# Optimization experiments

Measured on AMD Instinct MI355X. Metric: run time of the kernel, lower is better.

Reference implementation:

```python
import jax, jax.numpy as jnp
import numpy as np

NEG_POS_RATIO = 3
BETA = 1.0
ALPHA = 2.0


def _smooth_ex_loss(pred, tgt):
    # a = beta / (1 - exp(-alpha)); c = a - beta - beta/alpha
    a = BETA / (1.0 - np.exp(-ALPHA))
    c = a - BETA - BETA / ALPHA
    diff = jnp.abs(pred - tgt)
    return jnp.where(diff < 1.0,
                     a * (diff + (jnp.exp(-ALPHA * diff) - 1.0) / ALPHA),
                     BETA * diff + c)


def setup_inputs() -> dict:
    key = jax.random.key(0)
    k1, k2, k3, k4 = jax.random.split(key, 4)
    B, P, C = 128, 8732, 21
    return {
        "confidence": jax.random.normal(k1, (B, P, C), dtype=jnp.float32),
        "predicted_locations": jax.random.normal(k2, (B, P, 4), dtype=jnp.float32),
        "labels": jax.random.randint(k3, (B, P), 0, C, dtype=jnp.int64),
        "gt_locations": jax.random.normal(k4, (B, P, 4), dtype=jnp.float32),
    }


def reference(confidence, predicted_locations, labels, gt_locations):
    # confidence: [B, P, C]; labels: [B, P]; locations: [B, P, 4]
    logp = jax.nn.log_softmax(confidence, axis=2)
    pos_mask = labels > 0

    # --- hard negative mining (no-grad in original) ---
    bg_loss = jax.lax.stop_gradient(-logp[:, :, 0])          # [B, P]
    num_pos = pos_mask.sum(axis=1, keepdims=True)             # [B, 1]
    num_neg = num_pos * NEG_POS_RATIO
    mined = jnp.where(pos_mask, -jnp.inf, bg_loss)
    idx = jnp.argsort(-mined, axis=1)                         # descending sort
    orders = jnp.argsort(idx, axis=1)                         # rank of each prior
    neg_mask = orders < num_neg
    mask = pos_mask | neg_mask                                # [B, P]

    # --- classification loss: sum of CE over mined priors ---
    per_elem_ce = -jnp.take_along_axis(logp, labels[..., None], axis=2)[..., 0]
    classification_loss = jnp.sum(jnp.where(mask, per_elem_ce, 0.0))

    # --- localization loss: smooth-ex loss over positive priors ---
    loc = _smooth_ex_loss(predicted_locations, gt_locations)  # [B, P, 4]
    smooth_sum = jnp.sum(jnp.where(pos_mask[..., None], loc, 0.0))

    n_pos_total = pos_mask.sum().astype(jnp.float32)
    return (smooth_sum / n_pos_total, classification_loss / n_pos_total)
```

## Files before the change

### kernel.cpp

```cpp
#include <hip/hip_runtime.h>
#include <cstdint>


#define B_ 128
#define P_ 8732
#define C_ 21
constexpr int BPR = 16;
constexpr int TPB = 256;
constexpr int GRID = B_ * BPR;
constexpr int TPR = BPR * TPB;

typedef float f32x4u __attribute__((ext_vector_type(4), aligned(4)));

__device__ __forceinline__ float waveSumF(float v) {
#pragma unroll
  for (int o = 32; o; o >>= 1) v += __shfl_down(v, o);
  return v;
}
__device__ __forceinline__ int waveSumI(int v) {
#pragma unroll
  for (int o = 32; o; o >>= 1) v += __shfl_down(v, o);
  return v;
}
__device__ __forceinline__ double waveSumD(double v) {
#pragma unroll
  for (int o = 32; o; o >>= 1) v += __shfl_down(v, o);
  return v;
}

#define SMEX(d) (((d) < 1.f) ? (1.1565176427496657f * ((d) + (__expf(-2.f * (d)) - 1.f) * 0.5f)) \
                             : ((d) - 0.3434823572503343f))

__device__ __forceinline__ void doPrior(
    f32x4u v0, f32x4u v1, f32x4u v2, f32x4u v3, f32x4u v4, float t20,
    int lab, float4 pr, float4 gv, bool act,
    float& sm, float& cp, float& cn, int& np) {
  float m = fmaxf(fmaxf(fmaxf(v0.x, v0.y), fmaxf(v0.z, v0.w)),
                  fmaxf(fmaxf(v1.x, v1.y), fmaxf(v1.z, v1.w)));
  m = fmaxf(m, fmaxf(fmaxf(v2.x, v2.y), fmaxf(v2.z, v2.w)));
  m = fmaxf(m, fmaxf(fmaxf(v3.x, v3.y), fmaxf(v3.z, v3.w)));
  m = fmaxf(m, fmaxf(fmaxf(v4.x, v4.y), fmaxf(v4.z, v4.w)));
  m = fmaxf(m, t20);
  float s = __expf(v0.x - m) + __expf(v0.y - m) + __expf(v0.z - m) + __expf(v0.w - m);
  s += __expf(v1.x - m) + __expf(v1.y - m) + __expf(v1.z - m) + __expf(v1.w - m);
  s += __expf(v2.x - m) + __expf(v2.y - m) + __expf(v2.z - m) + __expf(v2.w - m);
  s += __expf(v3.x - m) + __expf(v3.y - m) + __expf(v3.z - m) + __expf(v3.w - m);
  s += __expf(v4.x - m) + __expf(v4.y - m) + __expf(v4.z - m) + __expf(v4.w - m);
  s += __expf(t20 - m);
  float xl = v0.x;
  xl = (lab == 1) ? v0.y : xl;  xl = (lab == 2) ? v0.z : xl;
  xl = (lab == 3) ? v0.w : xl;  xl = (lab == 4) ? v1.x : xl;
  xl = (lab == 5) ? v1.y : xl;  xl = (lab == 6) ? v1.z : xl;
  xl = (lab == 7) ? v1.w : xl;  xl = (lab == 8) ? v2.x : xl;
  xl = (lab == 9) ? v2.y : xl;  xl = (lab == 10) ? v2.z : xl;
  xl = (lab == 11) ? v2.w : xl; xl = (lab == 12) ? v3.x : xl;
  xl = (lab == 13) ? v3.y : xl; xl = (lab == 14) ? v3.z : xl;
  xl = (lab == 15) ? v3.w : xl; xl = (lab == 16) ? v4.x : xl;
  xl = (lab == 17) ? v4.y : xl; xl = (lab == 18) ? v4.z : xl;
  xl = (lab == 19) ? v4.w : xl; xl = (lab == 20) ? t20 : xl;
  const float ce = m + __logf(s) - xl;

  float d, smx;
  d = fabsf(pr.x - gv.x); smx = SMEX(d);
  d = fabsf(pr.y - gv.y); smx += SMEX(d);
  d = fabsf(pr.z - gv.z); smx += SMEX(d);
  d = fabsf(pr.w - gv.w); smx += SMEX(d);

  const bool pos = act && (lab > 0);
  sm += pos ? smx : 0.f;
  cp += pos ? ce : 0.f;
  cn += (act && lab == 0) ? ce : 0.f;
  np += pos ? 1 : 0;
}

__global__ __launch_bounds__(TPB, 2) void k_main(
    const float* __restrict__ conf, const float* __restrict__ pred,
    const int* __restrict__ labels, const float* __restrict__ gt,
    float4* __restrict__ part) {
  const int tid = threadIdx.x;
  const int row = blockIdx.x >> 4;
  const int sub = blockIdx.x & 15;
  const int p0 = sub * TPB + tid;
  const int p1 = p0 + TPR;
  const int p2 = p0 + 2 * TPR;
  const bool act2 = p2 < P_;
  const int p2c = act2 ? p2 : p0;
  const size_t rb = (size_t)row * P_;
  const float4* pred4 = (const float4*)pred;
  const float4* gt4 = (const float4*)gt;

  const f32x4u* q0 = (const f32x4u*)(conf + (rb + p0) * C_);
  const f32x4u* q1 = (const f32x4u*)(conf + (rb + p1) * C_);
  const f32x4u* q2 = (const f32x4u*)(conf + (rb + p2c) * C_);
  const f32x4u a0 = q0[0], a1 = q0[1], a2 = q0[2], a3 = q0[3], a4 = q0[4];
  const f32x4u b0 = q1[0], b1 = q1[1], b2 = q1[2], b3 = q1[3], b4 = q1[4];
  const f32x4u c0 = q2[0], c1 = q2[1], c2 = q2[2], c3 = q2[3], c4 = q2[4];
  const float a5 = ((const float*)q0)[20];
  const float b5 = ((const float*)q1)[20];
  const float c5 = ((const float*)q2)[20];
  const int la = labels[rb + p0], lb = labels[rb + p1], lc = labels[rb + p2c];
  const float4 pra = pred4[rb + p0], prb = pred4[rb + p1], prc = pred4[rb + p2c];
  const float4 gva = gt4[rb + p0], gvb = gt4[rb + p1], gvc = gt4[rb + p2c];

  float sm = 0.f, cp = 0.f, cn = 0.f;
  int np = 0;
  doPrior(a0, a1, a2, a3, a4, a5, la, pra, gva, true, sm, cp, cn, np);
  doPrior(b0, b1, b2, b3, b4, b5, lb, prb, gvb, true, sm, cp, cn, np);
  doPrior(c0, c1, c2, c3, c4, c5, lc, prc, gvc, act2, sm, cp, cn, np);

  float r0 = waveSumF(sm), r1 = waveSumF(cp), r2 = waveSumF(cn);
  int r3 = waveSumI(np);
  __shared__ float s0[4], s1[4], s2[4];
  __shared__ int s3[4];
  const int wid = tid >> 6, lane = tid & 63;
  if (lane == 0) { s0[wid] = r0; s1[wid] = r1; s2[wid] = r2; s3[wid] = r3; }
  __syncthreads();
  if (tid == 0) {
    part[blockIdx.x] = make_float4(
        s0[0] + s0[1] + s0[2] + s0[3], s1[0] + s1[1] + s1[2] + s1[3],
        s2[0] + s2[1] + s2[2] + s2[3], (float)(s3[0] + s3[1] + s3[2] + s3[3]));
  }
}

__device__ __forceinline__ unsigned keyCE(const float* __restrict__ conf,
                                          const int* __restrict__ labels,
                                          int b, int p, float& ce) {
  const float* row = conf + ((size_t)b * P_ + p) * C_;
  float m = row[0];
  for (int c = 1; c < C_; ++c) m = fmaxf(m, row[c]);
  float s = 0.f;
  for (int c = 0; c < C_; ++c) s += __expf(row[c] - m);
  const float lse = m + __logf(s);
  const int lab = labels[(size_t)b * P_ + p];
  ce = lse - row[lab];
  if (lab > 0) return 0u;
  unsigned u = __float_as_uint(lse - row[0]);
  u = (u & 0x80000000u) ? ~u : (u | 0x80000000u);
  return u ? u : 1u;
}

__global__ __launch_bounds__(128) void k_tail(
    const float4* __restrict__ part, const float* __restrict__ conf,
    const int* __restrict__ labels, float* __restrict__ out) {
  const int tid = threadIdx.x;
  const int wid = tid >> 6, lane = tid & 63;
  __shared__ int s_np[B_], s_flag[B_];
  __shared__ double sdA[2], sdB[2], sdC[2];
  __shared__ int siN[2];
  __shared__ double s_extra;
  __shared__ int icnt[2];
  __shared__ float fsum[2];

  double sm = 0.0, cp = 0.0, cnSel = 0.0;
  int npr = 0;
  {
    double cn = 0.0;
#pragma unroll
    for (int i = 0; i < BPR; ++i) {
      const float4 v = part[tid * BPR + i];
      sm += (double)v.x;
      cp += (double)v.y;
      cn += (double)v.z;
      npr += (int)v.w;
    }
    s_np[tid] = npr;
    const int fl = (3 * npr < P_ - npr) ? 1 : 0;
    s_flag[tid] = fl;
    if (!fl) cnSel = cn;
  }
  const double t1 = waveSumD(sm), t2 = waveSumD(cp), t3 = waveSumD(cnSel);
  const int t4 = waveSumI(npr);
  if (lane == 0) { sdA[wid] = t1; sdB[wid] = t2; sdC[wid] = t3; siN[wid] = t4; }
  if (tid == 0) s_extra = 0.0;
  __syncthreads();

  for (int b = 0; b < B_; ++b) {
    if (!s_flag[b]) continue;
    const int need = 3 * s_np[b];
    unsigned long long lo = 1, hi = 0xFFFFFFFFull, ans = 1;
    while (lo <= hi) {
      const unsigned long long mid = lo + ((hi - lo) >> 1);
      int c = 0;
      float dummy;
      for (int p = tid; p < P_; p += 128)
        if ((unsigned long long)keyCE(conf, labels, b, p, dummy) >= mid) c++;
      c = waveSumI(c);
      if (lane == 0) icnt[wid] = c;
      __syncthreads();
      const int tot = icnt[0] + icnt[1];
      if (tot >= need) { ans = mid; lo = mid + 1; } else { hi = mid - 1; }
      __syncthreads();
    }
    int cgt = 0;
    float sgt = 0.f;
    for (int p = tid; p < P_; p += 128) {
      float ce;
      const unsigned long long k = keyCE(conf, labels, b, p, ce);
      if (k > ans) { cgt++; sgt += ce; }
    }
    cgt = waveSumI(cgt);
    sgt = waveSumF(sgt);
    if (lane == 0) { icnt[wid] = cgt; fsum[wid] = sgt; }
    __syncthreads();
    if (tid == 0) {
      const int gtot = icnt[0] + icnt[1];
      double s = (double)(fsum[0] + fsum[1]);
      int rm = need - gtot;
      int taken = 0;
      for (int p = 0; p < P_ && taken < rm; ++p) {
        float ce;
        if (keyCE(conf, labels, b, p, ce) == ans) { s += ce; taken++; }
      }
      s_extra += s;
    }
    __syncthreads();
  }

  if (tid == 0) {
    const double G0 = sdA[0] + sdA[1];
    const double G1 = sdB[0] + sdB[1];
    const double G2 = sdC[0] + sdC[1] + s_extra;
    const double N = (double)(siN[0] + siN[1]);
    out[0] = (float)(G0 / N);
    out[1] = (float)((G1 + G2) / N);
  }
}

extern "C" void kernel_launch(void* const* d_in, const int* in_sizes, int n_in,
                              void* d_out, int out_size, void* d_ws, size_t ws_size,
                              hipStream_t stream) {
  const float* conf = (const float*)d_in[0];
  const float* pred = (const float*)d_in[1];
  const int* labels = (const int*)d_in[2];
  const float* gt = (const float*)d_in[3];
  float* out = (float*)d_out;

  float4* part = (float4*)d_ws;

  hipLaunchKernelGGL(k_main, dim3(GRID), dim3(TPB), 0, stream,
                     conf, pred, labels, gt, part);
  hipLaunchKernelGGL(k_tail, dim3(1), dim3(128), 0, stream,
                     part, conf, labels, out);
}
```

Measured before the change: 39.23 us.

## Fuse main and tail kernels via last-block-done atomic counter with inline-asm loads

Merges the per-block partial-sum kernel and the single-block tail kernel into one launch. Each block publishes its partials with atomic stores, and the block that increments a global counter last performs the final reduction and the hard-negative mining. All loads are issued up front as inline-asm global_load instructions followed by one explicit waitcnt, to maximise memory-level parallelism. This removes a kernel launch and its gap, and the tail now runs with 256 threads instead of 128. In exchange it relies on the counter wrapping modulo GRID across calls, since the workspace is never reset. It also drops the launch_bounds occupancy hint of 2.

```diff
diff --git a/kernel.cpp b/kernel.cpp
--- a/kernel.cpp
+++ b/kernel.cpp
@@ -5,12 +5,16 @@
 #define B_ 128
 #define P_ 8732
 #define C_ 21
+constexpr int TPB = 256;
 constexpr int BPR = 16;
-constexpr int TPB = 256;
 constexpr int GRID = B_ * BPR;
 constexpr int TPR = BPR * TPB;
 
-typedef float f32x4u __attribute__((ext_vector_type(4), aligned(4)));
+typedef float f4 __attribute__((ext_vector_type(4)));
+
+#define LD4(d, a, o) asm volatile("global_load_dwordx4 %0, %1, off offset:" #o : "=v"(d) : "v"(a))
+#define LDF(d, a, o) asm volatile("global_load_dword %0, %1, off offset:" #o : "=v"(d) : "v"(a))
+#define LDI(d, a)    asm volatile("global_load_dword %0, %1, off" : "=v"(d) : "v"(a))
 
 __device__ __forceinline__ float waveSumF(float v) {
 #pragma unroll
@@ -31,33 +35,32 @@
 #define SMEX(d) (((d) < 1.f) ? (1.1565176427496657f * ((d) + (__expf(-2.f * (d)) - 1.f) * 0.5f)) \
                              : ((d) - 0.3434823572503343f))
 
-__device__ __forceinline__ void doPrior(
-    f32x4u v0, f32x4u v1, f32x4u v2, f32x4u v3, f32x4u v4, float t20,
-    int lab, float4 pr, float4 gv, bool act,
-    float& sm, float& cp, float& cn, int& np) {
-  float m = fmaxf(fmaxf(fmaxf(v0.x, v0.y), fmaxf(v0.z, v0.w)),
-                  fmaxf(fmaxf(v1.x, v1.y), fmaxf(v1.z, v1.w)));
-  m = fmaxf(m, fmaxf(fmaxf(v2.x, v2.y), fmaxf(v2.z, v2.w)));
-  m = fmaxf(m, fmaxf(fmaxf(v3.x, v3.y), fmaxf(v3.z, v3.w)));
-  m = fmaxf(m, fmaxf(fmaxf(v4.x, v4.y), fmaxf(v4.z, v4.w)));
-  m = fmaxf(m, t20);
-  float s = __expf(v0.x - m) + __expf(v0.y - m) + __expf(v0.z - m) + __expf(v0.w - m);
-  s += __expf(v1.x - m) + __expf(v1.y - m) + __expf(v1.z - m) + __expf(v1.w - m);
-  s += __expf(v2.x - m) + __expf(v2.y - m) + __expf(v2.z - m) + __expf(v2.w - m);
-  s += __expf(v3.x - m) + __expf(v3.y - m) + __expf(v3.z - m) + __expf(v3.w - m);
-  s += __expf(v4.x - m) + __expf(v4.y - m) + __expf(v4.z - m) + __expf(v4.w - m);
-  s += __expf(t20 - m);
-  float xl = v0.x;
-  xl = (lab == 1) ? v0.y : xl;  xl = (lab == 2) ? v0.z : xl;
-  xl = (lab == 3) ? v0.w : xl;  xl = (lab == 4) ? v1.x : xl;
-  xl = (lab == 5) ? v1.y : xl;  xl = (lab == 6) ? v1.z : xl;
-  xl = (lab == 7) ? v1.w : xl;  xl = (lab == 8) ? v2.x : xl;
-  xl = (lab == 9) ? v2.y : xl;  xl = (lab == 10) ? v2.z : xl;
-  xl = (lab == 11) ? v2.w : xl; xl = (lab == 12) ? v3.x : xl;
-  xl = (lab == 13) ? v3.y : xl; xl = (lab == 14) ? v3.z : xl;
-  xl = (lab == 15) ? v3.w : xl; xl = (lab == 16) ? v4.x : xl;
-  xl = (lab == 17) ? v4.y : xl; xl = (lab == 18) ? v4.z : xl;
-  xl = (lab == 19) ? v4.w : xl; xl = (lab == 20) ? t20 : xl;
+__device__ __forceinline__ void prior21v(f4 c0, f4 c1, f4 c2, f4 c3, f4 c4, float c5,
+                                         int lab, f4 pr, f4 gv, bool act,
+                                         float& sm, float& cp, float& cn, int& np) {
+  float m = fmaxf(fmaxf(fmaxf(c0.x, c0.y), fmaxf(c0.z, c0.w)),
+                  fmaxf(fmaxf(c1.x, c1.y), fmaxf(c1.z, c1.w)));
+  m = fmaxf(m, fmaxf(fmaxf(c2.x, c2.y), fmaxf(c2.z, c2.w)));
+  m = fmaxf(m, fmaxf(fmaxf(c3.x, c3.y), fmaxf(c3.z, c3.w)));
+  m = fmaxf(m, fmaxf(fmaxf(c4.x, c4.y), fmaxf(c4.z, c4.w)));
+  m = fmaxf(m, c5);
+  float s = __expf(c0.x - m) + __expf(c0.y - m) + __expf(c0.z - m) + __expf(c0.w - m);
+  s += __expf(c1.x - m) + __expf(c1.y - m) + __expf(c1.z - m) + __expf(c1.w - m);
+  s += __expf(c2.x - m) + __expf(c2.y - m) + __expf(c2.z - m) + __expf(c2.w - m);
+  s += __expf(c3.x - m) + __expf(c3.y - m) + __expf(c3.z - m) + __expf(c3.w - m);
+  s += __expf(c4.x - m) + __expf(c4.y - m) + __expf(c4.z - m) + __expf(c4.w - m);
+  s += __expf(c5 - m);
+  float xl = c0.x;
+  xl = (lab == 1) ? c0.y : xl;  xl = (lab == 2) ? c0.z : xl;
+  xl = (lab == 3) ? c0.w : xl;  xl = (lab == 4) ? c1.x : xl;
+  xl = (lab == 5) ? c1.y : xl;  xl = (lab == 6) ? c1.z : xl;
+  xl = (lab == 7) ? c1.w : xl;  xl = (lab == 8) ? c2.x : xl;
+  xl = (lab == 9) ? c2.y : xl;  xl = (lab == 10) ? c2.z : xl;
+  xl = (lab == 11) ? c2.w : xl; xl = (lab == 12) ? c3.x : xl;
+  xl = (lab == 13) ? c3.y : xl; xl = (lab == 14) ? c3.z : xl;
+  xl = (lab == 15) ? c3.w : xl; xl = (lab == 16) ? c4.x : xl;
+  xl = (lab == 17) ? c4.y : xl; xl = (lab == 18) ? c4.z : xl;
+  xl = (lab == 19) ? c4.w : xl; xl = (lab == 20) ? c5 : xl;
   const float ce = m + __logf(s) - xl;
 
   float d, smx;
@@ -71,55 +74,6 @@
   cp += pos ? ce : 0.f;
   cn += (act && lab == 0) ? ce : 0.f;
   np += pos ? 1 : 0;
-}
-
-__global__ __launch_bounds__(TPB, 2) void k_main(
-    const float* __restrict__ conf, const float* __restrict__ pred,
-    const int* __restrict__ labels, const float* __restrict__ gt,
-    float4* __restrict__ part) {
-  const int tid = threadIdx.x;
-  const int row = blockIdx.x >> 4;
-  const int sub = blockIdx.x & 15;
-  const int p0 = sub * TPB + tid;
-  const int p1 = p0 + TPR;
-  const int p2 = p0 + 2 * TPR;
-  const bool act2 = p2 < P_;
-  const int p2c = act2 ? p2 : p0;
-  const size_t rb = (size_t)row * P_;
-  const float4* pred4 = (const float4*)pred;
-  const float4* gt4 = (const float4*)gt;
-
-  const f32x4u* q0 = (const f32x4u*)(conf + (rb + p0) * C_);
-  const f32x4u* q1 = (const f32x4u*)(conf + (rb + p1) * C_);
-  const f32x4u* q2 = (const f32x4u*)(conf + (rb + p2c) * C_);
-  const f32x4u a0 = q0[0], a1 = q0[1], a2 = q0[2], a3 = q0[3], a4 = q0[4];
-  const f32x4u b0 = q1[0], b1 = q1[1], b2 = q1[2], b3 = q1[3], b4 = q1[4];
-  const f32x4u c0 = q2[0], c1 = q2[1], c2 = q2[2], c3 = q2[3], c4 = q2[4];
-  const float a5 = ((const float*)q0)[20];
-  const float b5 = ((const float*)q1)[20];
-  const float c5 = ((const float*)q2)[20];
-  const int la = labels[rb + p0], lb = labels[rb + p1], lc = labels[rb + p2c];
-  const float4 pra = pred4[rb + p0], prb = pred4[rb + p1], prc = pred4[rb + p2c];
-  const float4 gva = gt4[rb + p0], gvb = gt4[rb + p1], gvc = gt4[rb + p2c];
-
-  float sm = 0.f, cp = 0.f, cn = 0.f;
-  int np = 0;
-  doPrior(a0, a1, a2, a3, a4, a5, la, pra, gva, true, sm, cp, cn, np);
-  doPrior(b0, b1, b2, b3, b4, b5, lb, prb, gvb, true, sm, cp, cn, np);
-  doPrior(c0, c1, c2, c3, c4, c5, lc, prc, gvc, act2, sm, cp, cn, np);
-
-  float r0 = waveSumF(sm), r1 = waveSumF(cp), r2 = waveSumF(cn);
-  int r3 = waveSumI(np);
-  __shared__ float s0[4], s1[4], s2[4];
-  __shared__ int s3[4];
-  const int wid = tid >> 6, lane = tid & 63;
-  if (lane == 0) { s0[wid] = r0; s1[wid] = r1; s2[wid] = r2; s3[wid] = r3; }
-  __syncthreads();
-  if (tid == 0) {
-    part[blockIdx.x] = make_float4(
-        s0[0] + s0[1] + s0[2] + s0[3], s1[0] + s1[1] + s1[2] + s1[3],
-        s2[0] + s2[1] + s2[2] + s2[3], (float)(s3[0] + s3[1] + s3[2] + s3[3]));
-  }
 }
 
 __device__ __forceinline__ unsigned keyCE(const float* __restrict__ conf,
@@ -139,37 +93,110 @@
   return u ? u : 1u;
 }
 
-__global__ __launch_bounds__(128) void k_tail(
-    const float4* __restrict__ part, const float* __restrict__ conf,
-    const int* __restrict__ labels, float* __restrict__ out) {
+union F2U {
+  float2 f;
+  unsigned long long u;
+};
+
+__global__ __launch_bounds__(TPB) void k_fused(
+    const float* __restrict__ conf, const float* __restrict__ pred,
+    const int* __restrict__ labels, const float* __restrict__ gt,
+    unsigned long long* __restrict__ slots, unsigned* __restrict__ cnt,
+    float* __restrict__ out) {
   const int tid = threadIdx.x;
+  const int row = blockIdx.x >> 4;
+  const int sub = blockIdx.x & 15;
+  const int p0 = sub * TPB + tid;
+  const int p1 = p0 + TPR;
+  const int p2 = p0 + 2 * TPR;
+  const bool act2 = p2 < P_;
+  const int p2c = act2 ? p2 : p0;
+  const size_t rb = (size_t)row * P_;
+
+  const uint64_t ca0 = (uint64_t)(conf + (rb + p0) * C_);
+  const uint64_t ca1 = (uint64_t)(conf + (rb + p1) * C_);
+  const uint64_t ca2 = (uint64_t)(conf + (rb + (size_t)p2c) * C_);
+  const uint64_t la0 = (uint64_t)(labels + rb + p0);
+  const uint64_t la1 = (uint64_t)(labels + rb + p1);
+  const uint64_t la2 = (uint64_t)(labels + rb + p2c);
+  const uint64_t pa0 = (uint64_t)(pred + (rb + p0) * 4);
+  const uint64_t pa1 = (uint64_t)(pred + (rb + p1) * 4);
+  const uint64_t pa2 = (uint64_t)(pred + (rb + (size_t)p2c) * 4);
+  const uint64_t ga0 = (uint64_t)(gt + (rb + p0) * 4);
+  const uint64_t ga1 = (uint64_t)(gt + (rb + p1) * 4);
+  const uint64_t ga2 = (uint64_t)(gt + (rb + (size_t)p2c) * 4);
+
+  f4 A0, A1, A2, A3, A4, B0, B1, B2, B3, B4, C0, C1, C2, C3, C4;
+  float A5, B5, C5;
+  int LA, LB, LC;
+  f4 PA, PB, PC, GA, GB, GC;
+  LD4(A0, ca0, 0); LD4(A1, ca0, 16); LD4(A2, ca0, 32); LD4(A3, ca0, 48); LD4(A4, ca0, 64); LDF(A5, ca0, 80);
+  LD4(B0, ca1, 0); LD4(B1, ca1, 16); LD4(B2, ca1, 32); LD4(B3, ca1, 48); LD4(B4, ca1, 64); LDF(B5, ca1, 80);
+  LD4(C0, ca2, 0); LD4(C1, ca2, 16); LD4(C2, ca2, 32); LD4(C3, ca2, 48); LD4(C4, ca2, 64); LDF(C5, ca2, 80);
+  LDI(LA, la0); LDI(LB, la1); LDI(LC, la2);
+  LD4(PA, pa0, 0); LD4(PB, pa1, 0); LD4(PC, pa2, 0);
+  LD4(GA, ga0, 0); LD4(GB, ga1, 0); LD4(GC, ga2, 0);
+
+  asm volatile("s_waitcnt vmcnt(0)" ::: "memory");
+  __builtin_amdgcn_sched_barrier(0);
+
+  float sm = 0.f, cp = 0.f, cn = 0.f;
+  int np = 0;
+  prior21v(A0, A1, A2, A3, A4, A5, LA, PA, GA, true, sm, cp, cn, np);
+  prior21v(B0, B1, B2, B3, B4, B5, LB, PB, GB, true, sm, cp, cn, np);
+  prior21v(C0, C1, C2, C3, C4, C5, LC, PC, GC, act2, sm, cp, cn, np);
+
+  const float r0 = waveSumF(sm), r1 = waveSumF(cp), r2 = waveSumF(cn);
+  const int r3 = waveSumI(np);
+  __shared__ float s0[4], s1[4], s2[4];
+  __shared__ int s3[4];
+  __shared__ int s_win;
   const int wid = tid >> 6, lane = tid & 63;
+  if (lane == 0) { s0[wid] = r0; s1[wid] = r1; s2[wid] = r2; s3[wid] = r3; }
+  __syncthreads();
+  if (tid == 0) {
+    F2U w0, w1;
+    w0.f = make_float2(s0[0] + s0[1] + s0[2] + s0[3], s1[0] + s1[1] + s1[2] + s1[3]);
+    w1.f = make_float2(s2[0] + s2[1] + s2[2] + s2[3], (float)(s3[0] + s3[1] + s3[2] + s3[3]));
+    __hip_atomic_store(&slots[2 * blockIdx.x], w0.u, __ATOMIC_RELAXED, __HIP_MEMORY_SCOPE_AGENT);
+    __hip_atomic_store(&slots[2 * blockIdx.x + 1], w1.u, __ATOMIC_RELAXED, __HIP_MEMORY_SCOPE_AGENT);
+    __threadfence();
+    const unsigned old = __hip_atomic_fetch_add(cnt, 1u, __ATOMIC_ACQ_REL, __HIP_MEMORY_SCOPE_AGENT);
+    s_win = ((old & (GRID - 1)) == (GRID - 1)) ? 1 : 0;
+  }
+  __syncthreads();
+  if (!s_win) return;
+
+  __threadfence();
   __shared__ int s_np[B_], s_flag[B_];
-  __shared__ double sdA[2], sdB[2], sdC[2];
-  __shared__ int siN[2];
+  __shared__ double sdA[4], sdB[4], sdC[4];
+  __shared__ int siN[4];
   __shared__ double s_extra;
-  __shared__ int icnt[2];
-  __shared__ float fsum[2];
-
-  double sm = 0.0, cp = 0.0, cnSel = 0.0;
-  int npr = 0;
-  {
-    double cn = 0.0;
+  __shared__ int icnt[4];
+  __shared__ float fsum[4];
+
+  double smR = 0.0, cpR = 0.0, cnSel = 0.0;
+  int npR = 0;
+  if (tid < B_) {
+    double cnR = 0.0;
 #pragma unroll
     for (int i = 0; i < BPR; ++i) {
-      const float4 v = part[tid * BPR + i];
-      sm += (double)v.x;
-      cp += (double)v.y;
-      cn += (double)v.z;
-      npr += (int)v.w;
-    }
-    s_np[tid] = npr;
-    const int fl = (3 * npr < P_ - npr) ? 1 : 0;
+      const int sidx = tid * BPR + i;
+      F2U a, b;
+      a.u = __hip_atomic_load(&slots[2 * sidx], __ATOMIC_RELAXED, __HIP_MEMORY_SCOPE_AGENT);
+      b.u = __hip_atomic_load(&slots[2 * sidx + 1], __ATOMIC_RELAXED, __HIP_MEMORY_SCOPE_AGENT);
+      smR += (double)a.f.x;
+      cpR += (double)a.f.y;
+      cnR += (double)b.f.x;
+      npR += (int)b.f.y;
+    }
+    s_np[tid] = npR;
+    const int fl = (3 * npR < P_ - npR) ? 1 : 0;
     s_flag[tid] = fl;
-    if (!fl) cnSel = cn;
-  }
-  const double t1 = waveSumD(sm), t2 = waveSumD(cp), t3 = waveSumD(cnSel);
-  const int t4 = waveSumI(npr);
+    if (!fl) cnSel = cnR;
+  }
+  const double t1 = waveSumD(smR), t2 = waveSumD(cpR), t3 = waveSumD(cnSel);
+  const int t4 = waveSumI(npR);
   if (lane == 0) { sdA[wid] = t1; sdB[wid] = t2; sdC[wid] = t3; siN[wid] = t4; }
   if (tid == 0) s_extra = 0.0;
   __syncthreads();
@@ -182,18 +209,18 @@
       const unsigned long long mid = lo + ((hi - lo) >> 1);
       int c = 0;
       float dummy;
-      for (int p = tid; p < P_; p += 128)
+      for (int p = tid; p < P_; p += TPB)
         if ((unsigned long long)keyCE(conf, labels, b, p, dummy) >= mid) c++;
       c = waveSumI(c);
       if (lane == 0) icnt[wid] = c;
       __syncthreads();
-      const int tot = icnt[0] + icnt[1];
+      const int tot = icnt[0] + icnt[1] + icnt[2] + icnt[3];
       if (tot >= need) { ans = mid; lo = mid + 1; } else { hi = mid - 1; }
       __syncthreads();
     }
     int cgt = 0;
     float sgt = 0.f;
-    for (int p = tid; p < P_; p += 128) {
+    for (int p = tid; p < P_; p += TPB) {
       float ce;
       const unsigned long long k = keyCE(conf, labels, b, p, ce);
       if (k > ans) { cgt++; sgt += ce; }
@@ -203,24 +230,24 @@
     if (lane == 0) { icnt[wid] = cgt; fsum[wid] = sgt; }
     __syncthreads();
     if (tid == 0) {
-      const int gtot = icnt[0] + icnt[1];
-      double s = (double)(fsum[0] + fsum[1]);
+      const int gtot = icnt[0] + icnt[1] + icnt[2] + icnt[3];
+      double sx = (double)(fsum[0] + fsum[1] + fsum[2] + fsum[3]);
       int rm = need - gtot;
       int taken = 0;
       for (int p = 0; p < P_ && taken < rm; ++p) {
         float ce;
-        if (keyCE(conf, labels, b, p, ce) == ans) { s += ce; taken++; }
+        if (keyCE(conf, labels, b, p, ce) == ans) { sx += ce; taken++; }
       }
-      s_extra += s;
+      s_extra += sx;
     }
     __syncthreads();
   }
 
   if (tid == 0) {
-    const double G0 = sdA[0] + sdA[1];
-    const double G1 = sdB[0] + sdB[1];
-    const double G2 = sdC[0] + sdC[1] + s_extra;
-    const double N = (double)(siN[0] + siN[1]);
+    const double G0 = sdA[0] + sdA[1] + sdA[2] + sdA[3];
+    const double G1 = sdB[0] + sdB[1] + sdB[2] + sdB[3];
+    const double G2 = sdC[0] + sdC[1] + sdC[2] + sdC[3] + s_extra;
+    const double N = (double)(siN[0] + siN[1] + siN[2] + siN[3]);
     out[0] = (float)(G0 / N);
     out[1] = (float)((G1 + G2) / N);
   }
@@ -235,10 +262,9 @@
   const float* gt = (const float*)d_in[3];
   float* out = (float*)d_out;
 
-  float4* part = (float4*)d_ws;
-
-  hipLaunchKernelGGL(k_main, dim3(GRID), dim3(TPB), 0, stream,
-                     conf, pred, labels, gt, part);
-  hipLaunchKernelGGL(k_tail, dim3(1), dim3(128), 0, stream,
-                     part, conf, labels, out);
-}
+  unsigned long long* slots = (unsigned long long*)d_ws;
+  unsigned* cnt = (unsigned*)(slots + 2 * GRID);
+
+  hipLaunchKernelGGL(k_fused, dim3(GRID), dim3(TPB), 0, stream,
+                     conf, pred, labels, gt, slots, cnt, out);
+}
```

Result: slower. 144.5 us (+268.3%).
